# Performance work log

Measured on AMD Instinct MI355X. Metric: run time of the kernel, lower is better.

## Reference

```python
import jax, jax.numpy as jnp
import numpy as np

N_NODES = 100000
N_EDGES = 1600000
N_REL = 4


def rgcn_conv(x, src, dst, edge_type, W, root, bias):
    """PyG RGCNConv with default aggr='mean': out_i = x_i @ root + bias
    + sum_r mean_{j in N_r(i)} (x_j @ W_r)."""
    n = x.shape[0]
    num_rel = W.shape[0]
    out_dim = W.shape[2]
    # Transform all nodes by every relation weight first (small dims -> cheap),
    # avoiding a huge [E, in, out] gathered-weight tensor.
    xW = jnp.einsum('nd,rdo->rno', x, W)          # [R, N, out]
    msg = xW[edge_type, src]                      # [E, out] gather
    seg = edge_type.astype(jnp.int32) * n + dst   # composite (relation, dst) id
    num_seg = num_rel * n
    sums = jax.ops.segment_sum(msg, seg, num_segments=num_seg)            # [R*N, out]
    cnt = jax.ops.segment_sum(jnp.ones_like(seg, dtype=x.dtype), seg,
                              num_segments=num_seg)                        # [R*N]
    mean = sums / jnp.maximum(cnt, 1.0)[:, None]
    agg = mean.reshape(num_rel, n, out_dim).sum(axis=0)                    # [N, out]
    return agg + x @ root + bias


def setup_inputs() -> dict:
    key = jax.random.key(0)
    ks = jax.random.split(key, 12)
    inp = {}
    inp['x'] = jax.random.normal(ks[0], (N_NODES, 16), dtype=jnp.float32)
    inp['edge_index'] = jax.random.randint(ks[1], (2, N_EDGES), 0, N_NODES, dtype=jnp.int32)
    inp['edge_type'] = jax.random.randint(ks[2], (N_EDGES,), 0, N_REL, dtype=jnp.int32)
    dims = [(16, 16), (16, 32), (32, 64)]
    for i, (din, dout) in enumerate(dims, start=1):
        scale = 1.0 / np.sqrt(din)
        inp[f'W{i}'] = jax.random.normal(ks[3 * i], (N_REL, din, dout), dtype=jnp.float32) * scale
        inp[f'root{i}'] = jax.random.normal(ks[3 * i + 1], (din, dout), dtype=jnp.float32) * scale
        inp[f'b{i}'] = jnp.zeros((dout,), dtype=jnp.float32)
    return inp


def reference(x, edge_index, edge_type, W1, root1, b1, W2, root2, b2, W3, root3, b3):
    src, dst = edge_index[0], edge_index[1]
    h = rgcn_conv(x, src, dst, edge_type, W1, root1, b1)
    h = jax.nn.relu(h)  # dropout is identity in eval mode
    h = rgcn_conv(h, src, dst, edge_type, W2, root2, b2)
    h = jax.nn.relu(h)
    h = rgcn_conv(h, src, dst, edge_type, W3, root3, b3)
    return h
```

## Files before the change

kernel.cpp:

```cpp
#include <hip/hip_runtime.h>

#define N_NODES 100000
#define N_EDGES 1600000
#define N_REL 4
#define CAP 32

__global__ __launch_bounds__(256) void count_fill_kernel(
    const int* __restrict__ src, const int* __restrict__ dst,
    const int* __restrict__ et, int* __restrict__ cnt, int* __restrict__ elist,
    int E, int N) {
  int e = blockIdx.x * blockDim.x + threadIdx.x;
  if (e >= E) return;
  int seg = et[e] * N + dst[e];
  int pos = atomicAdd(&cnt[seg], 1);
  if (pos < CAP) elist[(long)seg * CAP + pos] = src[e];
}

template <int DIN, int DOUT, bool RELU>
__global__ __launch_bounds__(256, 8) void gather_transform_kernel(
    const float* __restrict__ x, const int* __restrict__ cnt,
    const int* __restrict__ elist, const float* __restrict__ W,
    const float* __restrict__ root, const float* __restrict__ bias,
    float* __restrict__ out, int N) {
  constexpr int G = DIN / 4;
  constexpr int GN = 256 / (N_REL * G);
  __shared__ float sAgg[GN][N_REL][DIN];
  __shared__ float sX[GN][DIN];

  {
    const int g = threadIdx.x % G;
    const int r = (threadIdx.x / G) % N_REL;
    const int ni = threadIdx.x / (G * N_REL);
    const int node = blockIdx.x * GN + ni;
    if (node < N) {
      const float4* xv = (const float4*)x;
      if (r == 0) {
        ((float4*)&sX[ni][0])[g] = xv[(long)node * G + g];
      }
      const int seg = r * N + node;
      int c = cnt[seg];
      c = c < CAP ? c : CAP;
      const int* el = elist + (long)seg * CAP;
      float4 s = {0.f, 0.f, 0.f, 0.f};
      int e = 0;
      for (; e + 2 <= c; e += 2) {
        int s0 = el[e], s1 = el[e + 1];
        float4 v0 = xv[(long)s0 * G + g];
        float4 v1 = xv[(long)s1 * G + g];
        s.x += v0.x + v1.x;
        s.y += v0.y + v1.y;
        s.z += v0.z + v1.z;
        s.w += v0.w + v1.w;
      }
      if (e < c) {
        float4 v0 = xv[(long)el[e] * G + g];
        s.x += v0.x;
        s.y += v0.y;
        s.z += v0.z;
        s.w += v0.w;
      }
      const float ic = (c > 0) ? 1.f / (float)c : 0.f;
      float4 m;
      m.x = s.x * ic;
      m.y = s.y * ic;
      m.z = s.z * ic;
      m.w = s.w * ic;
      ((float4*)&sAgg[ni][r][0])[g] = m;
    }
  }
  __syncthreads();

  constexpr int NPP = 256 / DOUT;
  constexpr int PASSES = GN / NPP;
  const int oc = threadIdx.x % DOUT;
  const int nj0 = threadIdx.x / DOUT;
#pragma unroll
  for (int p = 0; p < PASSES; p++) {
    const int nj = nj0 + p * NPP;
    const int node2 = blockIdx.x * GN + nj;
    if (node2 < N) {
      float acc = bias[oc];
#pragma unroll
      for (int k = 0; k < DIN; k++) acc += sX[nj][k] * root[k * DOUT + oc];
#pragma unroll
      for (int r = 0; r < N_REL; r++) {
#pragma unroll
        for (int k = 0; k < DIN; k++)
          acc += sAgg[nj][r][k] * W[(r * DIN + k) * DOUT + oc];
      }
      if (RELU) acc = fmaxf(acc, 0.f);
      out[(long)node2 * DOUT + oc] = acc;
    }
  }
}

static inline size_t align256(size_t v) { return (v + 255) & ~(size_t)255; }

extern "C" void kernel_launch(void* const* d_in, const int* in_sizes, int n_in,
                              void* d_out, int out_size, void* d_ws,
                              size_t ws_size, hipStream_t stream) {
  const int N = N_NODES;
  const int E = N_EDGES;
  const int RN = N_REL * N;

  const float* x = (const float*)d_in[0];
  const int* edge_index = (const int*)d_in[1];
  const int* et = (const int*)d_in[2];
  const float* W1 = (const float*)d_in[3];
  const float* root1 = (const float*)d_in[4];
  const float* b1 = (const float*)d_in[5];
  const float* W2 = (const float*)d_in[6];
  const float* root2 = (const float*)d_in[7];
  const float* b2 = (const float*)d_in[8];
  const float* W3 = (const float*)d_in[9];
  const float* root3 = (const float*)d_in[10];
  const float* b3 = (const float*)d_in[11];

  const int* src = edge_index;
  const int* dst = edge_index + E;

  char* ws = (char*)d_ws;
  size_t off = 0;
  int* cnt = (int*)(ws + off);
  off = align256(off + (size_t)RN * 4);
  int* elist = (int*)(ws + off);
  off = align256(off + (size_t)RN * CAP * 4);
  float* h1 = (float*)(ws + off);
  off = align256(off + (size_t)N * 16 * 4);
  float* h2 = (float*)(ws + off);
  off = align256(off + (size_t)N * 32 * 4);
  (void)ws_size;

  float* out = (float*)d_out;

  hipMemsetAsync(cnt, 0, (size_t)RN * 4, stream);
  count_fill_kernel<<<(E + 255) / 256, 256, 0, stream>>>(src, dst, et, cnt,
                                                         elist, E, N);

  {
    constexpr int GN = 256 / (N_REL * 4);
    gather_transform_kernel<16, 16, true>
        <<<(N + GN - 1) / GN, 256, 0, stream>>>(x, cnt, elist, W1, root1, b1,
                                                h1, N);
  }
  {
    constexpr int GN = 256 / (N_REL * 4);
    gather_transform_kernel<16, 32, true>
        <<<(N + GN - 1) / GN, 256, 0, stream>>>(h1, cnt, elist, W2, root2, b2,
                                                h2, N);
  }
  {
    constexpr int GN = 256 / (N_REL * 8);
    gather_transform_kernel<32, 64, false>
        <<<(N + GN - 1) / GN, 256, 0, stream>>>(h2, cnt, elist, W3, root3, b3,
                                                out, N);
  }
}
```

Before: 463.6 us.

## Switch to compact CSR edge lists and fp16 node features for gathers

Replaces the fixed-capacity padded per-segment edge lists with a compact CSR layout. It is built by a count pass, a block-scan allocation using an atomic top counter, and a fill pass. Node features and intermediate activations are stored in fp16, which halves the bytes moved by the random neighbour gathers, and accumulation stays in fp32. The gain in gather bandwidth comes at the cost of extra kernel launches, a second atomic pass over the edges, and reduced precision in the stored activations. Segments are no longer truncated at 32 entries.

```diff
diff --git a/kernel.cpp b/kernel.cpp
--- a/kernel.cpp
+++ b/kernel.cpp
@@ -1,28 +1,74 @@
 #include <hip/hip_runtime.h>
+#include <hip/hip_fp16.h>
 
 #define N_NODES 100000
 #define N_EDGES 1600000
 #define N_REL 4
-#define CAP 32
-
-__global__ __launch_bounds__(256) void count_fill_kernel(
+
+__global__ __launch_bounds__(256) void cvt_kernel(const float* __restrict__ in,
+                                                  __half* __restrict__ out,
+                                                  int n4) {
+  int i = blockIdx.x * 256 + threadIdx.x;
+  if (i >= n4) return;
+  float4 v = ((const float4*)in)[i];
+  __half2* o = (__half2*)(out + (long)i * 4);
+  o[0] = __floats2half2_rn(v.x, v.y);
+  o[1] = __floats2half2_rn(v.z, v.w);
+}
+
+__global__ __launch_bounds__(256) void count_kernel(const int* __restrict__ dst,
+                                                    const int* __restrict__ et,
+                                                    int* __restrict__ cnt,
+                                                    int E, int N) {
+  int e = blockIdx.x * 256 + threadIdx.x;
+  if (e >= E) return;
+  atomicAdd(&cnt[et[e] * N + dst[e]], 1);
+}
+
+__global__ __launch_bounds__(256) void alloc_kernel(const int* __restrict__ cnt,
+                                                    int* __restrict__ off,
+                                                    int* __restrict__ cur,
+                                                    int* __restrict__ top,
+                                                    int RN) {
+  __shared__ int s[256];
+  __shared__ int base;
+  const int i = blockIdx.x * 256 + threadIdx.x;
+  const int c = (i < RN) ? cnt[i] : 0;
+  s[threadIdx.x] = c;
+  __syncthreads();
+  for (int d = 1; d < 256; d <<= 1) {
+    int v = (threadIdx.x >= d) ? s[threadIdx.x - d] : 0;
+    __syncthreads();
+    s[threadIdx.x] += v;
+    __syncthreads();
+  }
+  if (threadIdx.x == 255) base = atomicAdd(top, s[255]);
+  __syncthreads();
+  if (i < RN) {
+    int excl = base + s[threadIdx.x] - c;
+    off[i] = excl;
+    cur[i] = excl;
+  }
+}
+
+__global__ __launch_bounds__(256) void fill_kernel(
     const int* __restrict__ src, const int* __restrict__ dst,
-    const int* __restrict__ et, int* __restrict__ cnt, int* __restrict__ elist,
+    const int* __restrict__ et, int* __restrict__ cur, int* __restrict__ eidx,
     int E, int N) {
-  int e = blockIdx.x * blockDim.x + threadIdx.x;
+  int e = blockIdx.x * 256 + threadIdx.x;
   if (e >= E) return;
   int seg = et[e] * N + dst[e];
-  int pos = atomicAdd(&cnt[seg], 1);
-  if (pos < CAP) elist[(long)seg * CAP + pos] = src[e];
-}
-
-template <int DIN, int DOUT, bool RELU>
+  int pos = atomicAdd(&cur[seg], 1);
+  eidx[pos] = src[e];
+}
+
+template <int DIN, int DOUT, bool RELU, bool OUT_HALF>
 __global__ __launch_bounds__(256, 8) void gather_transform_kernel(
-    const float* __restrict__ x, const int* __restrict__ cnt,
-    const int* __restrict__ elist, const float* __restrict__ W,
-    const float* __restrict__ root, const float* __restrict__ bias,
-    float* __restrict__ out, int N) {
-  constexpr int G = DIN / 4;
+    const __half* __restrict__ xh, const int* __restrict__ cnt,
+    const int* __restrict__ off, const int* __restrict__ eidx,
+    const float* __restrict__ W, const float* __restrict__ root,
+    const float* __restrict__ bias, void* __restrict__ outp, int N) {
+  constexpr int G = DIN / 8;
   constexpr int GN = 256 / (N_REL * G);
   __shared__ float sAgg[GN][N_REL][DIN];
   __shared__ float sX[GN][DIN];
@@ -33,39 +79,50 @@
     const int ni = threadIdx.x / (G * N_REL);
     const int node = blockIdx.x * GN + ni;
     if (node < N) {
-      const float4* xv = (const float4*)x;
+      const float4* xv = (const float4*)xh;
       if (r == 0) {
-        ((float4*)&sX[ni][0])[g] = xv[(long)node * G + g];
+        union { float4 f; __half2 h[4]; } u;
+        u.f = xv[(long)node * G + g];
+        float* d = &sX[ni][g * 8];
+#pragma unroll
+        for (int k = 0; k < 4; k++) {
+          float2 f2 = __half22float2(u.h[k]);
+          d[2 * k] = f2.x;
+          d[2 * k + 1] = f2.y;
+        }
       }
       const int seg = r * N + node;
-      int c = cnt[seg];
-      c = c < CAP ? c : CAP;
-      const int* el = elist + (long)seg * CAP;
-      float4 s = {0.f, 0.f, 0.f, 0.f};
+      const int c = cnt[seg];
+      const int st = off[seg];
+      float s[8] = {0.f, 0.f, 0.f, 0.f, 0.f, 0.f, 0.f, 0.f};
       int e = 0;
       for (; e + 2 <= c; e += 2) {
-        int s0 = el[e], s1 = el[e + 1];
-        float4 v0 = xv[(long)s0 * G + g];
-        float4 v1 = xv[(long)s1 * G + g];
-        s.x += v0.x + v1.x;
-        s.y += v0.y + v1.y;
-        s.z += v0.z + v1.z;
-        s.w += v0.w + v1.w;
+        int s0 = eidx[st + e], s1 = eidx[st + e + 1];
+        union { float4 f; __half2 h[4]; } u0, u1;
+        u0.f = xv[(long)s0 * G + g];
+        u1.f = xv[(long)s1 * G + g];
+#pragma unroll
+        for (int k = 0; k < 4; k++) {
+          float2 a = __half22float2(u0.h[k]);
+          float2 b = __half22float2(u1.h[k]);
+          s[2 * k] += a.x + b.x;
+          s[2 * k + 1] += a.y + b.y;
+        }
       }
       if (e < c) {
-        float4 v0 = xv[(long)el[e] * G + g];
-        s.x += v0.x;
-        s.y += v0.y;
-        s.z += v0.z;
-        s.w += v0.w;
+        union { float4 f; __half2 h[4]; } u0;
+        u0.f = xv[(long)eidx[st + e] * G + g];
+#pragma unroll
+        for (int k = 0; k < 4; k++) {
+          float2 a = __half22float2(u0.h[k]);
+          s[2 * k] += a.x;
+          s[2 * k + 1] += a.y;
+        }
       }
       const float ic = (c > 0) ? 1.f / (float)c : 0.f;
-      float4 m;
-      m.x = s.x * ic;
-      m.y = s.y * ic;
-      m.z = s.z * ic;
-      m.w = s.w * ic;
-      ((float4*)&sAgg[ni][r][0])[g] = m;
+      float* d = &sAgg[ni][r][g * 8];
+#pragma unroll
+      for (int k = 0; k < 8; k++) d[k] = s[k] * ic;
     }
   }
   __syncthreads();
@@ -89,7 +146,10 @@
           acc += sAgg[nj][r][k] * W[(r * DIN + k) * DOUT + oc];
       }
       if (RELU) acc = fmaxf(acc, 0.f);
-      out[(long)node2 * DOUT + oc] = acc;
+      if (OUT_HALF)
+        ((__half*)outp)[(long)node2 * DOUT + oc] = __float2half(acc);
+      else
+        ((float*)outp)[(long)node2 * DOUT + oc] = acc;
     }
   }
 }
@@ -120,39 +180,51 @@
   const int* dst = edge_index + E;
 
   char* ws = (char*)d_ws;
-  size_t off = 0;
-  int* cnt = (int*)(ws + off);
-  off = align256(off + (size_t)RN * 4);
-  int* elist = (int*)(ws + off);
-  off = align256(off + (size_t)RN * CAP * 4);
-  float* h1 = (float*)(ws + off);
-  off = align256(off + (size_t)N * 16 * 4);
-  float* h2 = (float*)(ws + off);
-  off = align256(off + (size_t)N * 32 * 4);
+  size_t off_b = 0;
+  int* cnt = (int*)(ws + off_b);
+  off_b = align256(off_b + (size_t)RN * 4);
+  int* off = (int*)(ws + off_b);
+  off_b = align256(off_b + (size_t)RN * 4);
+  int* cur = (int*)(ws + off_b);
+  off_b = align256(off_b + (size_t)RN * 4);
+  int* top = (int*)(ws + off_b);
+  off_b = align256(off_b + 256);
+  int* eidx = (int*)(ws + off_b);
+  off_b = align256(off_b + (size_t)E * 4);
+  __half* xh = (__half*)(ws + off_b);
+  off_b = align256(off_b + (size_t)N * 16 * 2);
+  __half* h1 = (__half*)(ws + off_b);
+  off_b = align256(off_b + (size_t)N * 16 * 2);
+  __half* h2 = (__half*)(ws + off_b);
+  off_b = align256(off_b + (size_t)N * 32 * 2);
   (void)ws_size;
 
   float* out = (float*)d_out;
 
   hipMemsetAsync(cnt, 0, (size_t)RN * 4, stream);
-  count_fill_kernel<<<(E + 255) / 256, 256, 0, stream>>>(src, dst, et, cnt,
-                                                         elist, E, N);
-
+  hipMemsetAsync(top, 0, 256, stream);
+  cvt_kernel<<<(N * 16 / 4 + 255) / 256, 256, 0, stream>>>(x, xh, N * 16 / 4);
+  count_kernel<<<(E + 255) / 256, 256, 0, stream>>>(dst, et, cnt, E, N);
+  alloc_kernel<<<(RN + 255) / 256, 256, 0, stream>>>(cnt, off, cur, top, RN);
+  fill_kernel<<<(E + 255) / 256, 256, 0, stream>>>(src, dst, et, cur, eidx, E,
+                                                   N);
+
+  {
+    constexpr int GN = 256 / (N_REL * 2);
+    gather_transform_kernel<16, 16, true, true>
+        <<<(N + GN - 1) / GN, 256, 0, stream>>>(xh, cnt, off, eidx, W1, root1,
+                                                b1, h1, N);
+  }
+  {
+    constexpr int GN = 256 / (N_REL * 2);
+    gather_transform_kernel<16, 32, true, true>
+        <<<(N + GN - 1) / GN, 256, 0, stream>>>(h1, cnt, off, eidx, W2, root2,
+                                                b2, h2, N);
+  }
   {
     constexpr int GN = 256 / (N_REL * 4);
-    gather_transform_kernel<16, 16, true>
-        <<<(N + GN - 1) / GN, 256, 0, stream>>>(x, cnt, elist, W1, root1, b1,
-                                                h1, N);
-  }
-  {
-    constexpr int GN = 256 / (N_REL * 4);
-    gather_transform_kernel<16, 32, true>
-        <<<(N + GN - 1) / GN, 256, 0, stream>>>(h1, cnt, elist, W2, root2, b2,
-                                                h2, N);
-  }
-  {
-    constexpr int GN = 256 / (N_REL * 8);
-    gather_transform_kernel<32, 64, false>
-        <<<(N + GN - 1) / GN, 256, 0, stream>>>(h2, cnt, elist, W3, root3, b3,
-                                                out, N);
-  }
-}
+    gather_transform_kernel<32, 64, false, false>
+        <<<(N + GN - 1) / GN, 256, 0, stream>>>(h2, cnt, off, eidx, W3, root3,
+                                                b3, out, N);
+  }
+}
```

New measurement: 516.5 us. +11.4%, slower.
